# Kernel optimization log

Hardware: AMD Instinct MI355X
Metric: run time of the kernel (lower is better)

## Reference

```python
import jax, jax.numpy as jnp
import numpy as np

B, R, S = 4, 16384, 96

def setup_inputs() -> dict:
    key = jax.random.key(0)
    k1, k2, k3, k4 = jax.random.split(key, 4)
    colors = jax.random.normal(k1, (B, R, S, 3), dtype=jnp.float32)
    densities = jax.random.normal(k2, (B, R, S, 1), dtype=jnp.float32)
    # depths must be monotonically increasing along the sample axis
    depths = jnp.sort(jax.random.uniform(k3, (B, R, S, 1), dtype=jnp.float32), axis=2)
    sample_coordinates = jax.random.uniform(k4, (B, R, S, 3), dtype=jnp.float32)
    return {"colors": colors, "densities": densities, "depths": depths,
            "sample_coordinates": sample_coordinates, "white_back": 0}


def reference(colors, densities, depths, sample_coordinates, white_back):
    deltas = depths[:, :, 1:] - depths[:, :, :-1]                     # [B,R,S-1,1]
    colors_mid = (colors[:, :, :-1] + colors[:, :, 1:]) * 0.5
    densities_mid = (densities[:, :, :-1] + densities[:, :, 1:]) * 0.5
    depths_mid = (depths[:, :, :-1] + depths[:, :, 1:]) * 0.5
    coords_mid = (sample_coordinates[:, :, :-1] + sample_coordinates[:, :, 1:]) * 0.5

    densities_mid = jax.nn.softplus(densities_mid)                    # activation_factory
    alpha = 1.0 - jnp.exp(-densities_mid * deltas)                    # [B,R,S-1,1]

    ones = jnp.ones_like(alpha[:, :, :1])
    alpha_shifted = jnp.concatenate([ones, 1.0 - alpha + 1e-10], axis=-2)
    trans = jnp.cumprod(alpha_shifted, axis=-2)[:, :, :-1]            # transmittance T_i

    weights = alpha * trans                                            # [B,R,S-1,1]
    tau = trans[:, :, -1, :]                                           # [B,R,1]

    composite_rgb = jnp.sum(weights * colors_mid, axis=-2)             # [B,R,3]
    composite_point = jnp.sum(weights * coords_mid, axis=-2)           # [B,R,3]
    weight_total = jnp.sum(weights, axis=2)                            # [B,R,1]

    composite_depth = jnp.sum(weights * depths_mid, axis=-2)           # [B,R,1]
    composite_depth = jnp.nan_to_num(composite_depth, nan=jnp.inf)
    composite_depth = jnp.clip(composite_depth, jnp.min(depths), jnp.max(depths))

    composite_rgb = jnp.where(white_back != 0,
                              composite_rgb + 1.0 - weight_total,
                              composite_rgb)
    return composite_rgb, composite_depth, weights, composite_point, tau
```

## Files before the change

### kernel.cpp

```cpp
#include <hip/hip_runtime.h>
#include <hip/hip_bf16.h>

#define NRAYS 65536
#define NS    96
#define NI    95

#define OFF_RGB   0
#define OFF_DEPTH 196608
#define OFF_W     262144
#define OFF_PT    6488064
#define OFF_TAU   6684672

__global__ void depth_minmax_full(const float* __restrict__ deps, unsigned* ws) {
    const int nt = gridDim.x * blockDim.x;
    int t = blockIdx.x * blockDim.x + threadIdx.x;
    float lo = __int_as_float(0x7f800000);
    float hi = 0.0f;
    const float4* Z4 = (const float4*)deps;
    const int n4 = NRAYS * NS / 4;
    for (int i = t; i < n4; i += nt) {
        float4 z = Z4[i];
        lo = fminf(lo, fminf(fminf(z.x, z.y), fminf(z.z, z.w)));
        hi = fmaxf(hi, fmaxf(fmaxf(z.x, z.y), fmaxf(z.z, z.w)));
    }
    #pragma unroll
    for (int off = 32; off; off >>= 1) {
        lo = fminf(lo, __shfl_xor(lo, off, 64));
        hi = fmaxf(hi, __shfl_xor(hi, off, 64));
    }
    if ((threadIdx.x & 63) == 0) {
        atomicMin(&ws[0], __float_as_uint(lo));
        atomicMax(&ws[1], __float_as_uint(hi));
    }
}

__device__ __forceinline__ float softplus_fast(float x) {
    return fmaxf(x, 0.0f) + __logf(1.0f + __expf(-fabsf(x)));
}

__launch_bounds__(256)
__global__ void raymarch(const float* __restrict__ colors,
                         const float* __restrict__ dens,
                         const float* __restrict__ deps,
                         const float* __restrict__ coords,
                         const int* __restrict__ wbp,
                         const unsigned* __restrict__ mm,
                         float* __restrict__ out) {
    const int lane = threadIdx.x & 63;
    const int g = blockIdx.x * 4 + (threadIdx.x >> 6);

    const bool v0 = (lane <= 47);
    const bool v1 = (lane <= 46);

    float2 dp = make_float2(0.f, 0.f);
    float2 dn = make_float2(0.f, 0.f);
    float2 c01 = make_float2(0.f, 0.f), c23 = make_float2(0.f, 0.f),
           c45 = make_float2(0.f, 0.f);
    float2 p01 = make_float2(0.f, 0.f), p23 = make_float2(0.f, 0.f),
           p45 = make_float2(0.f, 0.f);
    if (v0) {
        const float2* dpp = (const float2*)(deps + (size_t)g * NS);
        const float2* dnp = (const float2*)(dens + (size_t)g * NS);
        dp = dpp[lane];
        dn = dnp[lane];
        const float2* cp = (const float2*)(colors + (size_t)g * NS * 3);
        c01 = cp[3 * lane + 0]; c23 = cp[3 * lane + 1]; c45 = cp[3 * lane + 2];
        const float2* pp = (const float2*)(coords + (size_t)g * NS * 3);
        p01 = pp[3 * lane + 0]; p23 = pp[3 * lane + 1]; p45 = pp[3 * lane + 2];
    }
    const int src = (lane < 63) ? lane + 1 : 63;
    float d2  = __shfl(dp.x, src, 64);
    float n2  = __shfl(dn.x, src, 64);
    float cx2 = __shfl(c01.x, src, 64);
    float cy2 = __shfl(c01.y, src, 64);
    float cz2 = __shfl(c23.x, src, 64);
    float px2 = __shfl(p01.x, src, 64);
    float py2 = __shfl(p01.y, src, 64);
    float pz2 = __shfl(p23.x, src, 64);

    float E0 = __expf(-softplus_fast(0.5f * (dn.x + dn.y)) * (dp.y - dp.x));
    float a0 = v0 ? (1.0f - E0) : 0.0f;
    float f0 = v0 ? (E0 + 1e-10f) : 1.0f;
    float E1 = __expf(-softplus_fast(0.5f * (dn.y + n2)) * (d2 - dp.y));
    float a1 = v1 ? (1.0f - E1) : 0.0f;
    float f1 = v1 ? (E1 + 1e-10f) : 1.0f;

    float incl = f0 * f1;
    #pragma unroll
    for (int off = 1; off < 64; off <<= 1) {
        float t = __shfl_up(incl, off, 64);
        if (lane >= off) incl *= t;
    }
    float excl = __shfl_up(incl, 1, 64);
    if (lane == 0) excl = 1.0f;
    float w0 = a0 * excl;
    float w1 = a1 * (excl * f0);
    float tau = __shfl(excl, 47, 64);

    float dm0 = 0.5f * (dp.x + dp.y), dm1 = 0.5f * (dp.y + d2);
    float cm0x = 0.5f * (c01.x + c23.y), cm0y = 0.5f * (c01.y + c45.x), cm0z = 0.5f * (c23.x + c45.y);
    float cm1x = 0.5f * (c23.y + cx2),   cm1y = 0.5f * (c45.x + cy2),   cm1z = 0.5f * (c45.y + cz2);
    float pm0x = 0.5f * (p01.x + p23.y), pm0y = 0.5f * (p01.y + p45.x), pm0z = 0.5f * (p23.x + p45.y);
    float pm1x = 0.5f * (p23.y + px2),   pm1y = 0.5f * (p45.x + py2),   pm1z = 0.5f * (p45.y + pz2);

    {
        size_t wb = (size_t)OFF_W + (size_t)g * NI + 2 * lane;
        if (v0) out[wb]     = w0;
        if (v1) out[wb + 1] = w1;
    }

    float acc[8];
    acc[0] = w0 * cm0x + w1 * cm1x;
    acc[1] = w0 * cm0y + w1 * cm1y;
    acc[2] = w0 * cm0z + w1 * cm1z;
    acc[3] = w0 * pm0x + w1 * pm1x;
    acc[4] = w0 * pm0y + w1 * pm1y;
    acc[5] = w0 * pm0z + w1 * pm1z;
    acc[6] = w0 * dm0  + w1 * dm1;
    acc[7] = w0 + w1;
    #pragma unroll
    for (int k = 0; k < 8; ++k) {
        #pragma unroll
        for (int off = 32; off; off >>= 1)
            acc[k] += __shfl_xor(acc[k], off, 64);
    }

    if (lane == 0) {
        float add = (wbp != nullptr && wbp[0] != 0) ? (1.0f - acc[7]) : 0.0f;
        size_t rb = (size_t)OFF_RGB + (size_t)g * 3;
        out[rb + 0] = acc[0] + add;
        out[rb + 1] = acc[1] + add;
        out[rb + 2] = acc[2] + add;
        size_t pb = (size_t)OFF_PT + (size_t)g * 3;
        out[pb + 0] = acc[3];
        out[pb + 1] = acc[4];
        out[pb + 2] = acc[5];
        float cd = acc[6];
        if (cd != cd) cd = __int_as_float(0x7f800000);
        float dmin = __uint_as_float(mm[0]);
        float dmax = __uint_as_float(mm[1]);
        cd = fminf(fmaxf(cd, dmin), dmax);
        out[OFF_DEPTH + g] = cd;
        out[OFF_TAU + g]   = tau;
    }
}

extern "C" void kernel_launch(void* const* d_in, const int* in_sizes, int n_in,
                              void* d_out, int out_size, void* d_ws, size_t ws_size,
                              hipStream_t stream) {
    const float* colors = (const float*)d_in[0];
    const float* dens   = (const float*)d_in[1];
    const float* deps   = (const float*)d_in[2];
    const float* coords = (const float*)d_in[3];
    const int*   wb     = (n_in > 4) ? (const int*)d_in[4] : nullptr;
    float* out = (float*)d_out;
    unsigned* mm = (unsigned*)d_ws;

    hipMemsetAsync(mm, 0xFF, 4, stream);
    hipMemsetAsync(mm + 1, 0x00, 4, stream);
    depth_minmax_full<<<256, 256, 0, stream>>>(deps, mm);
    raymarch<<<NRAYS / 4, 256, 0, stream>>>(colors, dens, deps, coords, wb, mm, out);
}
```

Before: 244.9 us.

## Process rays with 16-lane groups and use sortedness for depth min/max

The raymarch kernel now assigns 16 lanes per ray with six samples each, instead of a full 64-lane wave per ray where a quarter of the lanes sat idle. This shortens the scan and reduction shuffle chains and does more serial work per thread. The depth min/max kernel now reads only the first and last sample of each ray, relying on depths being sorted along the sample axis. It also merges the two memsets into one by storing the max as an inverted atomicMin. The sortedness shortcut holds only if the inputs stay sorted, which the task guarantees.

```diff
diff --git a/kernel.cpp b/kernel.cpp
--- a/kernel.cpp
+++ b/kernel.cpp
@@ -1,5 +1,4 @@
 #include <hip/hip_runtime.h>
-#include <hip/hip_bf16.h>
 
 #define NRAYS 65536
 #define NS    96
@@ -11,18 +10,10 @@
 #define OFF_PT    6488064
 #define OFF_TAU   6684672
 
-__global__ void depth_minmax_full(const float* __restrict__ deps, unsigned* ws) {
-    const int nt = gridDim.x * blockDim.x;
-    int t = blockIdx.x * blockDim.x + threadIdx.x;
-    float lo = __int_as_float(0x7f800000);
-    float hi = 0.0f;
-    const float4* Z4 = (const float4*)deps;
-    const int n4 = NRAYS * NS / 4;
-    for (int i = t; i < n4; i += nt) {
-        float4 z = Z4[i];
-        lo = fminf(lo, fminf(fminf(z.x, z.y), fminf(z.z, z.w)));
-        hi = fmaxf(hi, fmaxf(fmaxf(z.x, z.y), fmaxf(z.z, z.w)));
-    }
+__global__ void depth_minmax_sorted(const float* __restrict__ deps, unsigned* ws) {
+    const int t = blockIdx.x * blockDim.x + threadIdx.x;
+    float lo = deps[(size_t)t * NS];
+    float hi = deps[(size_t)t * NS + (NS - 1)];
     #pragma unroll
     for (int off = 32; off; off >>= 1) {
         lo = fminf(lo, __shfl_xor(lo, off, 64));
@@ -30,7 +21,7 @@
     }
     if ((threadIdx.x & 63) == 0) {
         atomicMin(&ws[0], __float_as_uint(lo));
-        atomicMax(&ws[1], __float_as_uint(hi));
+        atomicMin(&ws[1], ~__float_as_uint(hi));
     }
 }
 
@@ -47,85 +38,95 @@
                          const unsigned* __restrict__ mm,
                          float* __restrict__ out) {
     const int lane = threadIdx.x & 63;
-    const int g = blockIdx.x * 4 + (threadIdx.x >> 6);
+    const int sub  = lane & 15;
+    const int g    = blockIdx.x * 16 + (threadIdx.x >> 4);
 
-    const bool v0 = (lane <= 47);
-    const bool v1 = (lane <= 46);
-
-    float2 dp = make_float2(0.f, 0.f);
-    float2 dn = make_float2(0.f, 0.f);
-    float2 c01 = make_float2(0.f, 0.f), c23 = make_float2(0.f, 0.f),
-           c45 = make_float2(0.f, 0.f);
-    float2 p01 = make_float2(0.f, 0.f), p23 = make_float2(0.f, 0.f),
-           p45 = make_float2(0.f, 0.f);
-    if (v0) {
-        const float2* dpp = (const float2*)(deps + (size_t)g * NS);
-        const float2* dnp = (const float2*)(dens + (size_t)g * NS);
-        dp = dpp[lane];
-        dn = dnp[lane];
-        const float2* cp = (const float2*)(colors + (size_t)g * NS * 3);
-        c01 = cp[3 * lane + 0]; c23 = cp[3 * lane + 1]; c45 = cp[3 * lane + 2];
-        const float2* pp = (const float2*)(coords + (size_t)g * NS * 3);
-        p01 = pp[3 * lane + 0]; p23 = pp[3 * lane + 1]; p45 = pp[3 * lane + 2];
+    float d[6], n[6], c[18], p[18];
+    {
+        const float2* q = (const float2*)(deps + (size_t)g * NS) + 3 * sub;
+        #pragma unroll
+        for (int j = 0; j < 3; ++j) { float2 v = q[j]; d[2*j] = v.x; d[2*j+1] = v.y; }
     }
-    const int src = (lane < 63) ? lane + 1 : 63;
-    float d2  = __shfl(dp.x, src, 64);
-    float n2  = __shfl(dn.x, src, 64);
-    float cx2 = __shfl(c01.x, src, 64);
-    float cy2 = __shfl(c01.y, src, 64);
-    float cz2 = __shfl(c23.x, src, 64);
-    float px2 = __shfl(p01.x, src, 64);
-    float py2 = __shfl(p01.y, src, 64);
-    float pz2 = __shfl(p23.x, src, 64);
-
-    float E0 = __expf(-softplus_fast(0.5f * (dn.x + dn.y)) * (dp.y - dp.x));
-    float a0 = v0 ? (1.0f - E0) : 0.0f;
-    float f0 = v0 ? (E0 + 1e-10f) : 1.0f;
-    float E1 = __expf(-softplus_fast(0.5f * (dn.y + n2)) * (d2 - dp.y));
-    float a1 = v1 ? (1.0f - E1) : 0.0f;
-    float f1 = v1 ? (E1 + 1e-10f) : 1.0f;
-
-    float incl = f0 * f1;
-    #pragma unroll
-    for (int off = 1; off < 64; off <<= 1) {
-        float t = __shfl_up(incl, off, 64);
-        if (lane >= off) incl *= t;
+    {
+        const float2* q = (const float2*)(dens + (size_t)g * NS) + 3 * sub;
+        #pragma unroll
+        for (int j = 0; j < 3; ++j) { float2 v = q[j]; n[2*j] = v.x; n[2*j+1] = v.y; }
     }
-    float excl = __shfl_up(incl, 1, 64);
-    if (lane == 0) excl = 1.0f;
-    float w0 = a0 * excl;
-    float w1 = a1 * (excl * f0);
-    float tau = __shfl(excl, 47, 64);
-
-    float dm0 = 0.5f * (dp.x + dp.y), dm1 = 0.5f * (dp.y + d2);
-    float cm0x = 0.5f * (c01.x + c23.y), cm0y = 0.5f * (c01.y + c45.x), cm0z = 0.5f * (c23.x + c45.y);
-    float cm1x = 0.5f * (c23.y + cx2),   cm1y = 0.5f * (c45.x + cy2),   cm1z = 0.5f * (c45.y + cz2);
-    float pm0x = 0.5f * (p01.x + p23.y), pm0y = 0.5f * (p01.y + p45.x), pm0z = 0.5f * (p23.x + p45.y);
-    float pm1x = 0.5f * (p23.y + px2),   pm1y = 0.5f * (p45.x + py2),   pm1z = 0.5f * (p45.y + pz2);
-
     {
-        size_t wb = (size_t)OFF_W + (size_t)g * NI + 2 * lane;
-        if (v0) out[wb]     = w0;
-        if (v1) out[wb + 1] = w1;
+        const float2* q = (const float2*)(colors + (size_t)g * NS * 3) + 9 * sub;
+        #pragma unroll
+        for (int j = 0; j < 9; ++j) { float2 v = q[j]; c[2*j] = v.x; c[2*j+1] = v.y; }
+    }
+    {
+        const float2* q = (const float2*)(coords + (size_t)g * NS * 3) + 9 * sub;
+        #pragma unroll
+        for (int j = 0; j < 9; ++j) { float2 v = q[j]; p[2*j] = v.x; p[2*j+1] = v.y; }
     }
 
+    const int nsrc = (lane & 48) | ((sub + 1) & 15);
+    float d6  = __shfl(d[0], nsrc, 64);
+    float n6  = __shfl(n[0], nsrc, 64);
+    float cn0 = __shfl(c[0], nsrc, 64);
+    float cn1 = __shfl(c[1], nsrc, 64);
+    float cn2 = __shfl(c[2], nsrc, 64);
+    float pn0 = __shfl(p[0], nsrc, 64);
+    float pn1 = __shfl(p[1], nsrc, 64);
+    float pn2 = __shfl(p[2], nsrc, 64);
+
+    float a[6], f[6];
+    #pragma unroll
+    for (int i = 0; i < 6; ++i) {
+        float dn1 = (i < 5) ? d[i+1] : d6;
+        float nn1 = (i < 5) ? n[i+1] : n6;
+        float E = __expf(-softplus_fast(0.5f * (n[i] + nn1)) * (dn1 - d[i]));
+        const bool valid = (i < 5) || (sub < 15);
+        a[i] = valid ? (1.0f - E) : 0.0f;
+        f[i] = valid ? (E + 1e-10f) : 1.0f;
+    }
+
+    float incl = ((f[0] * f[1]) * (f[2] * f[3])) * (f[4] * f[5]);
+    #pragma unroll
+    for (int off = 1; off < 16; off <<= 1) {
+        float t = __shfl_up(incl, off, 16);
+        if (sub >= off) incl *= t;
+    }
+    float excl = __shfl_up(incl, 1, 16);
+    if (sub == 0) excl = 1.0f;
+
     float acc[8];
-    acc[0] = w0 * cm0x + w1 * cm1x;
-    acc[1] = w0 * cm0y + w1 * cm1y;
-    acc[2] = w0 * cm0z + w1 * cm1z;
-    acc[3] = w0 * pm0x + w1 * pm1x;
-    acc[4] = w0 * pm0y + w1 * pm1y;
-    acc[5] = w0 * pm0z + w1 * pm1z;
-    acc[6] = w0 * dm0  + w1 * dm1;
-    acc[7] = w0 + w1;
+    #pragma unroll
+    for (int k = 0; k < 8; ++k) acc[k] = 0.0f;
+    float t = excl;
+    float tauc = 0.0f;
+    const size_t wb = (size_t)OFF_W + (size_t)g * NI + 6 * sub;
+    #pragma unroll
+    for (int i = 0; i < 6; ++i) {
+        float w = a[i] * t;
+        if (i < 5 || sub < 15) out[wb + i] = w;
+        float dn1 = (i < 5) ? d[i+1] : d6;
+        float dm  = 0.5f * (d[i] + dn1);
+        float cmx = 0.5f * (c[3*i+0] + ((i < 5) ? c[3*i+3] : cn0));
+        float cmy = 0.5f * (c[3*i+1] + ((i < 5) ? c[3*i+4] : cn1));
+        float cmz = 0.5f * (c[3*i+2] + ((i < 5) ? c[3*i+5] : cn2));
+        float pmx = 0.5f * (p[3*i+0] + ((i < 5) ? p[3*i+3] : pn0));
+        float pmy = 0.5f * (p[3*i+1] + ((i < 5) ? p[3*i+4] : pn1));
+        float pmz = 0.5f * (p[3*i+2] + ((i < 5) ? p[3*i+5] : pn2));
+        acc[0] += w * cmx;  acc[1] += w * cmy;  acc[2] += w * cmz;
+        acc[3] += w * pmx;  acc[4] += w * pmy;  acc[5] += w * pmz;
+        acc[6] += w * dm;   acc[7] += w;
+        if (i == 4) tauc = t;
+        t *= f[i];
+    }
+    float tau = __shfl(tauc, (lane & 48) | 15, 64);
+
     #pragma unroll
     for (int k = 0; k < 8; ++k) {
         #pragma unroll
-        for (int off = 32; off; off >>= 1)
+        for (int off = 1; off < 16; off <<= 1)
             acc[k] += __shfl_xor(acc[k], off, 64);
     }
 
-    if (lane == 0) {
+    if (sub == 0) {
         float add = (wbp != nullptr && wbp[0] != 0) ? (1.0f - acc[7]) : 0.0f;
         size_t rb = (size_t)OFF_RGB + (size_t)g * 3;
         out[rb + 0] = acc[0] + add;
@@ -138,7 +139,7 @@
         float cd = acc[6];
         if (cd != cd) cd = __int_as_float(0x7f800000);
         float dmin = __uint_as_float(mm[0]);
-        float dmax = __uint_as_float(mm[1]);
+        float dmax = __uint_as_float(~mm[1]);
         cd = fminf(fmaxf(cd, dmin), dmax);
         out[OFF_DEPTH + g] = cd;
         out[OFF_TAU + g]   = tau;
@@ -156,8 +157,7 @@
     float* out = (float*)d_out;
     unsigned* mm = (unsigned*)d_ws;
 
-    hipMemsetAsync(mm, 0xFF, 4, stream);
-    hipMemsetAsync(mm + 1, 0x00, 4, stream);
-    depth_minmax_full<<<256, 256, 0, stream>>>(deps, mm);
-    raymarch<<<NRAYS / 4, 256, 0, stream>>>(colors, dens, deps, coords, wb, mm, out);
+    hipMemsetAsync(mm, 0xFF, 8, stream);
+    depth_minmax_sorted<<<NRAYS / 256, 256, 0, stream>>>(deps, mm);
+    raymarch<<<NRAYS / 16, 256, 0, stream>>>(colors, dens, deps, coords, wb, mm, out);
 }
```

After: 236.2 us (median of 2 runs). 3.5% less time.
